# Performance work log

Measured on AMD Instinct MI355X. Metric: run time of the kernel, lower is better.

The kernel has to match this reference:

```python
import jax, jax.numpy as jnp
import numpy as np

LABELS_NUM_COUNT = [500000, 120000, 80000, 45000, 30000, 250000, 15000, 9000,
                    60000, 7000, 180000, 22000, 11000, 95000, 5000, 40000]
B, W = 2097152, 16  # batch, num_classes


def _build_penalty_matrix():
    c = np.asarray(LABELS_NUM_COUNT, dtype=np.float32)
    P = np.maximum(c[:, None], c[None, :]) / (c[:, None] + c[None, :])
    np.fill_diagonal(P, 1.0)
    return jnp.asarray(P)  # [W, W]


def setup_inputs() -> dict:
    key = jax.random.key(0)
    k1, k2 = jax.random.split(key)
    predict = jax.random.normal(k1, (B, W), dtype=jnp.float32)
    target = jax.random.normal(k2, (B, W), dtype=jnp.float32)
    return {"predict": predict, "target": target,
            "penalty_matrix": _build_penalty_matrix()}


def reference(predict, target, penalty_matrix):
    # `logpredict` in the original is actually softmax(predict).
    probs = jax.nn.softmax(predict, axis=-1)              # [B, W]
    pre = jnp.argmax(predict, axis=-1)                    # [B] predicted class
    tar = jnp.argmax(target, axis=-1)                     # [B] target class
    # scatter_ writes 1 at the predicted slot, then the loop overwrites it with
    # penalty[tar, pre] on mismatch or 0 on match -> net weight is:
    w = jnp.where(pre == tar, jnp.float32(0.0), penalty_matrix[tar, pre])  # [B]
    # sum(onehot * probs, -1) == probs at the predicted class
    p_at_pre = jnp.take_along_axis(probs, pre[:, None], axis=-1)[:, 0]     # [B]
    return jnp.mean(w * p_at_pre)
```

## Files before the change

kernel.cpp:

```cpp
#include <hip/hip_runtime.h>

#define NROWS 2097152
#define W 16

__global__ __launch_bounds__(256) void cel_weight_kernel(
    const float* __restrict__ predict,
    const float* __restrict__ target,
    const float* __restrict__ penalty,
    float* __restrict__ out)
{
    __shared__ float s_pen[W * W];
    __shared__ float s_part[4];

    const int tid = threadIdx.x;
    if (tid < W * W) s_pen[tid] = penalty[tid];
    __syncthreads();

    float acc = 0.0f;
    const int stride = gridDim.x * blockDim.x;

    for (int r = blockIdx.x * blockDim.x + tid; r < NROWS; r += stride) {
        const float4* prow = (const float4*)(predict + (size_t)r * W);
        const float4* trow = (const float4*)(target + (size_t)r * W);
        float4 p0 = prow[0], p1 = prow[1], p2 = prow[2], p3 = prow[3];
        float4 t0 = trow[0], t1 = trow[1], t2 = trow[2], t3 = trow[3];

        float pv[W] = {p0.x, p0.y, p0.z, p0.w, p1.x, p1.y, p1.z, p1.w,
                       p2.x, p2.y, p2.z, p2.w, p3.x, p3.y, p3.z, p3.w};
        float tv[W] = {t0.x, t0.y, t0.z, t0.w, t1.x, t1.y, t1.z, t1.w,
                       t2.x, t2.y, t2.z, t2.w, t3.x, t3.y, t3.z, t3.w};

        float pmax = pv[0]; int pidx = 0;
        #pragma unroll
        for (int j = 1; j < W; ++j) {
            if (pv[j] > pmax) { pmax = pv[j]; pidx = j; }
        }
        float s = 0.0f;
        #pragma unroll
        for (int j = 0; j < W; ++j) s += __expf(pv[j] - pmax);

        float tmax = tv[0]; int tidx = 0;
        #pragma unroll
        for (int j = 1; j < W; ++j) {
            if (tv[j] > tmax) { tmax = tv[j]; tidx = j; }
        }

        float wgt = (pidx == tidx) ? 0.0f : s_pen[tidx * W + pidx];
        acc += wgt / s;
    }

    #pragma unroll
    for (int off = 32; off > 0; off >>= 1)
        acc += __shfl_down(acc, off);

    const int lane = tid & 63;
    const int wid  = tid >> 6;
    if (lane == 0) s_part[wid] = acc;
    __syncthreads();

    if (tid == 0) {
        float tot = s_part[0] + s_part[1] + s_part[2] + s_part[3];
        atomicAdd(out, tot * (1.0f / (float)NROWS));
    }
}

extern "C" void kernel_launch(void* const* d_in, const int* in_sizes, int n_in,
                              void* d_out, int out_size, void* d_ws, size_t ws_size,
                              hipStream_t stream)
{
    const float* predict = (const float*)d_in[0];
    const float* target  = (const float*)d_in[1];
    const float* penalty = (const float*)d_in[2];
    float* out = (float*)d_out;

    hipMemsetAsync(out, 0, sizeof(float) * out_size, stream);

    dim3 grid(2048), block(256);
    cel_weight_kernel<<<grid, block, 0, stream>>>(predict, target, penalty, out);
}
```

Measured before the change: 274.0 us.

## Split each row across four lanes with shuffle reductions for coalesced loads

Each row is now handled by a quad of four threads, each loading one float4 of predict and target, so adjacent lanes read contiguous memory instead of each thread reading a 64-byte row. The argmax and softmax denominator are combined across the quad with xor shuffles, keeping first-index tie-breaking. The grid is doubled to keep total threads per row count reasonable. This costs extra shuffle instructions and leaves three of four lanes idle during accumulation.

Result: slower. 287.8 us (+5.1%).

```diff
diff --git a/kernel.cpp b/kernel.cpp
--- a/kernel.cpp
+++ b/kernel.cpp
@@ -16,37 +16,50 @@
     if (tid < W * W) s_pen[tid] = penalty[tid];
     __syncthreads();
 
+    const int quad = tid & 3;
+    const int gthread = blockIdx.x * blockDim.x + tid;
+    const int q0 = gthread >> 2;
+    const int nquads = (gridDim.x * blockDim.x) >> 2;
+    const int jbase = quad * 4;
+
     float acc = 0.0f;
-    const int stride = gridDim.x * blockDim.x;
 
-    for (int r = blockIdx.x * blockDim.x + tid; r < NROWS; r += stride) {
-        const float4* prow = (const float4*)(predict + (size_t)r * W);
-        const float4* trow = (const float4*)(target + (size_t)r * W);
-        float4 p0 = prow[0], p1 = prow[1], p2 = prow[2], p3 = prow[3];
-        float4 t0 = trow[0], t1 = trow[1], t2 = trow[2], t3 = trow[3];
+    for (int row = q0; row < NROWS; row += nquads) {
+        const size_t off = (size_t)row * W + jbase;
+        float4 p = *(const float4*)(predict + off);
+        float4 t = *(const float4*)(target + off);
 
-        float pv[W] = {p0.x, p0.y, p0.z, p0.w, p1.x, p1.y, p1.z, p1.w,
-                       p2.x, p2.y, p2.z, p2.w, p3.x, p3.y, p3.z, p3.w};
-        float tv[W] = {t0.x, t0.y, t0.z, t0.w, t1.x, t1.y, t1.z, t1.w,
-                       t2.x, t2.y, t2.z, t2.w, t3.x, t3.y, t3.z, t3.w};
-
-        float pmax = pv[0]; int pidx = 0;
+        float pmax = p.x; int pidx = jbase;
+        if (p.y > pmax) { pmax = p.y; pidx = jbase + 1; }
+        if (p.z > pmax) { pmax = p.z; pidx = jbase + 2; }
+        if (p.w > pmax) { pmax = p.w; pidx = jbase + 3; }
         #pragma unroll
-        for (int j = 1; j < W; ++j) {
-            if (pv[j] > pmax) { pmax = pv[j]; pidx = j; }
-        }
-        float s = 0.0f;
-        #pragma unroll
-        for (int j = 0; j < W; ++j) s += __expf(pv[j] - pmax);
-
-        float tmax = tv[0]; int tidx = 0;
-        #pragma unroll
-        for (int j = 1; j < W; ++j) {
-            if (tv[j] > tmax) { tmax = tv[j]; tidx = j; }
+        for (int d = 1; d <= 2; d <<= 1) {
+            float om = __shfl_xor(pmax, d);
+            int   oi = __shfl_xor(pidx, d);
+            if (om > pmax || (om == pmax && oi < pidx)) { pmax = om; pidx = oi; }
         }
 
-        float wgt = (pidx == tidx) ? 0.0f : s_pen[tidx * W + pidx];
-        acc += wgt / s;
+        float lsum = __expf(p.x - pmax) + __expf(p.y - pmax)
+                   + __expf(p.z - pmax) + __expf(p.w - pmax);
+        lsum += __shfl_xor(lsum, 1);
+        lsum += __shfl_xor(lsum, 2);
+
+        float tmax = t.x; int tidx = jbase;
+        if (t.y > tmax) { tmax = t.y; tidx = jbase + 1; }
+        if (t.z > tmax) { tmax = t.z; tidx = jbase + 2; }
+        if (t.w > tmax) { tmax = t.w; tidx = jbase + 3; }
+        #pragma unroll
+        for (int d = 1; d <= 2; d <<= 1) {
+            float om = __shfl_xor(tmax, d);
+            int   oi = __shfl_xor(tidx, d);
+            if (om > tmax || (om == tmax && oi < tidx)) { tmax = om; tidx = oi; }
+        }
+
+        if (quad == 0) {
+            float wgt = (pidx == tidx) ? 0.0f : s_pen[tidx * W + pidx];
+            acc += wgt / lsum;
+        }
     }
 
     #pragma unroll
@@ -75,6 +88,6 @@
 
     hipMemsetAsync(out, 0, sizeof(float) * out_size, stream);
 
-    dim3 grid(2048), block(256);
+    dim3 grid(4096), block(256);
     cel_weight_kernel<<<grid, block, 0, stream>>>(predict, target, penalty, out);
 }
```

## Split each row across four lanes with DPP reductions and register prefetch

Applied to the files above, without the earlier changes.

Each row is now handled by a quad of four lanes, each loading one float4, so consecutive lanes read contiguous memory and the loads coalesce instead of each thread striding 64 bytes. Max, argmax and the exp-sum are combined across the quad with DPP lane swizzles, and every lane adds the row result, which is why the final scale is divided by four. The loop is fully unrolled over a fixed iteration count with double-buffered register prefetch, and the grid is raised to 4096 blocks with an occupancy hint. The cost is extra cross-lane instructions and redundant per-lane accumulation, plus hardcoded sizes that assume the row count divides evenly.

Result: slower. 283.4 us (+3.4%).

```diff
diff --git a/kernel.cpp b/kernel.cpp
--- a/kernel.cpp
+++ b/kernel.cpp
@@ -1,9 +1,23 @@
 #include <hip/hip_runtime.h>
 
-#define NROWS 2097152
-#define W 16
+#define NROWS    2097152
+#define W        16
+#define NBLOCKS  4096
+#define NTHREADS 256
+#define NQUADS   ((NBLOCKS * NTHREADS) / 4)
+#define ITERS    (NROWS / NQUADS)
 
-__global__ __launch_bounds__(256) void cel_weight_kernel(
+template <int CTRL>
+__device__ __forceinline__ float dpp_f(float x) {
+    int r = __builtin_amdgcn_update_dpp(0, __float_as_int(x), CTRL, 0xF, 0xF, true);
+    return __int_as_float(r);
+}
+template <int CTRL>
+__device__ __forceinline__ int dpp_i(int x) {
+    return __builtin_amdgcn_update_dpp(0, x, CTRL, 0xF, 0xF, true);
+}
+
+__global__ __launch_bounds__(256, 6) void cel_weight_kernel(
     const float* __restrict__ predict,
     const float* __restrict__ target,
     const float* __restrict__ penalty,
@@ -13,40 +27,63 @@
     __shared__ float s_part[4];
 
     const int tid = threadIdx.x;
-    if (tid < W * W) s_pen[tid] = penalty[tid];
+    s_pen[tid] = penalty[tid];
     __syncthreads();
 
+    const int quad  = tid & 3;
+    const int jbase = quad * 4;
+    const int q0    = (blockIdx.x * NTHREADS + tid) >> 2;
+
+    const float* pp = predict + (size_t)q0 * W + jbase;
+    const float* tp = target  + (size_t)q0 * W + jbase;
+    const size_t STEP = (size_t)NQUADS * W;
+
+    float4 P[2], T[2];
+    P[0] = *(const float4*)(pp);
+    T[0] = *(const float4*)(tp);
+    P[1] = *(const float4*)(pp + STEP);
+    T[1] = *(const float4*)(tp + STEP);
+
     float acc = 0.0f;
-    const int stride = gridDim.x * blockDim.x;
 
-    for (int r = blockIdx.x * blockDim.x + tid; r < NROWS; r += stride) {
-        const float4* prow = (const float4*)(predict + (size_t)r * W);
-        const float4* trow = (const float4*)(target + (size_t)r * W);
-        float4 p0 = prow[0], p1 = prow[1], p2 = prow[2], p3 = prow[3];
-        float4 t0 = trow[0], t1 = trow[1], t2 = trow[2], t3 = trow[3];
-
-        float pv[W] = {p0.x, p0.y, p0.z, p0.w, p1.x, p1.y, p1.z, p1.w,
-                       p2.x, p2.y, p2.z, p2.w, p3.x, p3.y, p3.z, p3.w};
-        float tv[W] = {t0.x, t0.y, t0.z, t0.w, t1.x, t1.y, t1.z, t1.w,
-                       t2.x, t2.y, t2.z, t2.w, t3.x, t3.y, t3.z, t3.w};
-
-        float pmax = pv[0]; int pidx = 0;
-        #pragma unroll
-        for (int j = 1; j < W; ++j) {
-            if (pv[j] > pmax) { pmax = pv[j]; pidx = j; }
-        }
-        float s = 0.0f;
-        #pragma unroll
-        for (int j = 0; j < W; ++j) s += __expf(pv[j] - pmax);
-
-        float tmax = tv[0]; int tidx = 0;
-        #pragma unroll
-        for (int j = 1; j < W; ++j) {
-            if (tv[j] > tmax) { tmax = tv[j]; tidx = j; }
+    #pragma unroll
+    for (int k = 0; k < ITERS; ++k) {
+        const float4 p = P[k & 1];
+        const float4 t = T[k & 1];
+        if (k + 2 < ITERS) {
+            P[k & 1] = *(const float4*)(pp + (size_t)(k + 2) * STEP);
+            T[k & 1] = *(const float4*)(tp + (size_t)(k + 2) * STEP);
         }
 
-        float wgt = (pidx == tidx) ? 0.0f : s_pen[tidx * W + pidx];
-        acc += wgt / s;
+        float m = fmaxf(fmaxf(p.x, p.y), fmaxf(p.z, p.w));
+        m = fmaxf(m, dpp_f<0xB1>(m));
+        m = fmaxf(m, dpp_f<0x4E>(m));
+        int li = 127;
+        li = (p.w == m) ? jbase + 3 : li;
+        li = (p.z == m) ? jbase + 2 : li;
+        li = (p.y == m) ? jbase + 1 : li;
+        li = (p.x == m) ? jbase     : li;
+        li = min(li, dpp_i<0xB1>(li));
+        li = min(li, dpp_i<0x4E>(li));
+
+        float e = __expf(p.x - m) + __expf(p.y - m)
+                + __expf(p.z - m) + __expf(p.w - m);
+        e += dpp_f<0xB1>(e);
+        e += dpp_f<0x4E>(e);
+
+        float tm = fmaxf(fmaxf(t.x, t.y), fmaxf(t.z, t.w));
+        tm = fmaxf(tm, dpp_f<0xB1>(tm));
+        tm = fmaxf(tm, dpp_f<0x4E>(tm));
+        int ti = 127;
+        ti = (t.w == tm) ? jbase + 3 : ti;
+        ti = (t.z == tm) ? jbase + 2 : ti;
+        ti = (t.y == tm) ? jbase + 1 : ti;
+        ti = (t.x == tm) ? jbase     : ti;
+        ti = min(ti, dpp_i<0xB1>(ti));
+        ti = min(ti, dpp_i<0x4E>(ti));
+
+        float wgt = (li == ti) ? 0.0f : s_pen[ti * W + li];
+        acc += wgt / e;
     }
 
     #pragma unroll
@@ -60,7 +97,7 @@
 
     if (tid == 0) {
         float tot = s_part[0] + s_part[1] + s_part[2] + s_part[3];
-        atomicAdd(out, tot * (1.0f / (float)NROWS));
+        atomicAdd(out, tot * (0.25f / (float)NROWS));
     }
 }
 
@@ -75,6 +112,6 @@
 
     hipMemsetAsync(out, 0, sizeof(float) * out_size, stream);
 
-    dim3 grid(2048), block(256);
+    dim3 grid(NBLOCKS), block(NTHREADS);
     cel_weight_kernel<<<grid, block, 0, stream>>>(predict, target, penalty, out);
 }
```

## Stream rows into LDS with async double-buffered loads and two-stage reduction

Applied to the files above, without the earlier changes.

Each wave now owns four contiguous 64-row chunks. It uses global_load_lds 16-byte async copies into double-buffered LDS, so the next chunk is fetched while the current one is computed. Global reads become fully coalesced per wave instead of 64-byte per-thread strided loads. The atomicAdd plus memset is replaced by per-block partials in the workspace and a small second reduction kernel. Costs are a 64KB-per-block LDS footprint, possible bank conflicts on the float4 LDS reads, and an extra kernel launch.

Measured after the change: 278.7 us. No clear change (+1.7%).

```diff
diff --git a/kernel.cpp b/kernel.cpp
--- a/kernel.cpp
+++ b/kernel.cpp
@@ -1,29 +1,77 @@
 #include <hip/hip_runtime.h>
 
-#define NROWS 2097152
-#define W 16
+#define NROWS    2097152
+#define W        16
+#define NBLOCKS  2048
+#define NTHREADS 256
+#define WPB      4
+#define CPW      4
+#define CROWS    64
+#define CBYTES   (CROWS * W * 4)
 
-__global__ __launch_bounds__(256) void cel_weight_kernel(
+__device__ __forceinline__ void async16(const void* g, void* l) {
+    __builtin_amdgcn_global_load_lds(
+        (const __attribute__((address_space(1))) void*)g,
+        (__attribute__((address_space(3))) void*)l, 16, 0, 0);
+}
+
+#define WAITVM(n) asm volatile("s_waitcnt vmcnt(" #n ")" ::: "memory")
+
+__device__ __forceinline__ void stage_chunk(const char* pSrc, const char* tSrc,
+                                            float* lp, float* lt, int lane) {
+    #pragma unroll
+    for (int i = 0; i < 4; ++i) {
+        async16(pSrc + i * 1024 + lane * 16, (char*)lp + i * 1024);
+        async16(tSrc + i * 1024 + lane * 16, (char*)lt + i * 1024);
+    }
+}
+
+__global__ __launch_bounds__(256, 2) void cel_weight_kernel(
     const float* __restrict__ predict,
     const float* __restrict__ target,
     const float* __restrict__ penalty,
-    float* __restrict__ out)
+    float* __restrict__ partials)
 {
+    __shared__ float sbuf[WPB][2][2][1024];
     __shared__ float s_pen[W * W];
-    __shared__ float s_part[4];
+    __shared__ float s_part[WPB];
 
-    const int tid = threadIdx.x;
-    if (tid < W * W) s_pen[tid] = penalty[tid];
+    const int tid  = threadIdx.x;
+    const int w    = tid >> 6;
+    const int lane = tid & 63;
+
+    s_pen[tid] = penalty[tid];
     __syncthreads();
 
+    const int gw = blockIdx.x * WPB + w;
+    const int c0 = gw * CPW;
+    const char* pB = (const char*)predict;
+    const char* tB = (const char*)target;
+
+    stage_chunk(pB + (size_t)c0 * CBYTES, tB + (size_t)c0 * CBYTES,
+                &sbuf[w][0][0][0], &sbuf[w][0][1][0], lane);
+    stage_chunk(pB + (size_t)(c0 + 1) * CBYTES, tB + (size_t)(c0 + 1) * CBYTES,
+                &sbuf[w][1][0][0], &sbuf[w][1][1][0], lane);
+
     float acc = 0.0f;
-    const int stride = gridDim.x * blockDim.x;
 
-    for (int r = blockIdx.x * blockDim.x + tid; r < NROWS; r += stride) {
-        const float4* prow = (const float4*)(predict + (size_t)r * W);
-        const float4* trow = (const float4*)(target + (size_t)r * W);
-        float4 p0 = prow[0], p1 = prow[1], p2 = prow[2], p3 = prow[3];
-        float4 t0 = trow[0], t1 = trow[1], t2 = trow[2], t3 = trow[3];
+    #pragma unroll
+    for (int k = 0; k < CPW; ++k) {
+        const int db = k & 1;
+        if (k < CPW - 1) { WAITVM(8); } else { WAITVM(0); }
+
+        const float* lp = &sbuf[w][db][0][lane * W];
+        const float* lt = &sbuf[w][db][1][lane * W];
+        float4 p0 = ((const float4*)lp)[0], p1 = ((const float4*)lp)[1],
+               p2 = ((const float4*)lp)[2], p3 = ((const float4*)lp)[3];
+        float4 t0 = ((const float4*)lt)[0], t1 = ((const float4*)lt)[1],
+               t2 = ((const float4*)lt)[2], t3 = ((const float4*)lt)[3];
+
+        if (k + 2 < CPW) {
+            const size_t c = (size_t)(c0 + k + 2);
+            stage_chunk(pB + c * CBYTES, tB + c * CBYTES,
+                        &sbuf[w][db][0][0], &sbuf[w][db][1][0], lane);
+        }
 
         float pv[W] = {p0.x, p0.y, p0.z, p0.w, p1.x, p1.y, p1.z, p1.w,
                        p2.x, p2.y, p2.z, p2.w, p3.x, p3.y, p3.z, p3.w};
@@ -32,18 +80,17 @@
 
         float pmax = pv[0]; int pidx = 0;
         #pragma unroll
-        for (int j = 1; j < W; ++j) {
+        for (int j = 1; j < W; ++j)
             if (pv[j] > pmax) { pmax = pv[j]; pidx = j; }
-        }
+
         float s = 0.0f;
         #pragma unroll
         for (int j = 0; j < W; ++j) s += __expf(pv[j] - pmax);
 
         float tmax = tv[0]; int tidx = 0;
         #pragma unroll
-        for (int j = 1; j < W; ++j) {
+        for (int j = 1; j < W; ++j)
             if (tv[j] > tmax) { tmax = tv[j]; tidx = j; }
-        }
 
         float wgt = (pidx == tidx) ? 0.0f : s_pen[tidx * W + pidx];
         acc += wgt / s;
@@ -52,16 +99,28 @@
     #pragma unroll
     for (int off = 32; off > 0; off >>= 1)
         acc += __shfl_down(acc, off);
+    if (lane == 0) s_part[w] = acc;
+    __syncthreads();
+    if (tid == 0)
+        partials[blockIdx.x] = s_part[0] + s_part[1] + s_part[2] + s_part[3];
+}
 
-    const int lane = tid & 63;
-    const int wid  = tid >> 6;
-    if (lane == 0) s_part[wid] = acc;
+__global__ __launch_bounds__(256) void reduce_kernel(
+    const float* __restrict__ partials, float* __restrict__ out)
+{
+    __shared__ float sp[4];
+    const int tid = threadIdx.x;
+    float a = 0.0f;
+    #pragma unroll
+    for (int i = 0; i < NBLOCKS / NTHREADS; ++i)
+        a += partials[tid + i * NTHREADS];
+    #pragma unroll
+    for (int off = 32; off > 0; off >>= 1)
+        a += __shfl_down(a, off);
+    if ((tid & 63) == 0) sp[tid >> 6] = a;
     __syncthreads();
-
-    if (tid == 0) {
-        float tot = s_part[0] + s_part[1] + s_part[2] + s_part[3];
-        atomicAdd(out, tot * (1.0f / (float)NROWS));
-    }
+    if (tid == 0)
+        out[0] = (sp[0] + sp[1] + sp[2] + sp[3]) * (1.0f / (float)NROWS);
 }
 
 extern "C" void kernel_launch(void* const* d_in, const int* in_sizes, int n_in,
@@ -71,10 +130,10 @@
     const float* predict = (const float*)d_in[0];
     const float* target  = (const float*)d_in[1];
     const float* penalty = (const float*)d_in[2];
-    float* out = (float*)d_out;
+    float* out      = (float*)d_out;
+    float* partials = (float*)d_ws;
 
-    hipMemsetAsync(out, 0, sizeof(float) * out_size, stream);
-
-    dim3 grid(2048), block(256);
-    cel_weight_kernel<<<grid, block, 0, stream>>>(predict, target, penalty, out);
+    cel_weight_kernel<<<dim3(NBLOCKS), dim3(NTHREADS), 0, stream>>>(
+        predict, target, penalty, partials);
+    reduce_kernel<<<dim3(1), dim3(NTHREADS), 0, stream>>>(partials, out);
 }
```
